# Performance work log

Measured on AMD Instinct MI355X. Metric: run time of the kernel, lower is better.

## Reference

```python
import jax, jax.numpy as jnp
import numpy as np

B, TOK, NT = 64, 64, 456          # batch, token_encoder_dim, num gene tokens
T = NT * TOK                      # flat gene_exp dim = 29184
D, H, NL = 256, 8, 4              # d_model, nhead, num_layers
HD = D // H                       # head_dim = 32
FF = 4 * D                        # ffn hidden
PH = 32                           # attention-pooling hidden
L = NT + 1                        # seq len incl. CLS token
LN_EPS = 1e-5
BN_EPS = 1e-5


def build_alibi_slopes(n_heads):
    # faithful to FlashAttentionBlock.build_alibi_slopes (base=2.0)
    return jnp.array([1.0 / 2.0 ** (i // (n_heads / 2.0)) for i in range(n_heads)],
                     dtype=jnp.float32)


def _ln(x, g, b):
    m = jnp.mean(x, axis=-1, keepdims=True)
    v = jnp.mean(jnp.square(x - m), axis=-1, keepdims=True)
    return (x - m) * jax.lax.rsqrt(v + LN_EPS) * g + b


def setup_inputs() -> dict:
    key = jax.random.key(0)
    ks = jax.random.split(key, 24)
    s = 0.02
    return {
        "gene_exp": jax.random.normal(ks[0], (B, T), dtype=jnp.float32),
        "coords": jax.random.normal(ks[1], (B, 3), dtype=jnp.float32),
        "w_in": jax.random.normal(ks[2], (TOK, D)) * s,
        "b_in": jnp.zeros((D,), jnp.float32),
        "w_cls": jax.random.normal(ks[3], (3, D)) * s,
        "b_cls": jnp.zeros((D,), jnp.float32),
        "qkv_w": jax.random.normal(ks[4], (NL, D, 3 * D)) * s,
        "qkv_b": jnp.zeros((NL, 3 * D), jnp.float32),
        "ln1_g": jnp.ones((NL, D), jnp.float32),
        "ln1_b": jnp.zeros((NL, D), jnp.float32),
        "ffn_w1": jax.random.normal(ks[5], (NL, D, FF)) * s,
        "ffn_b1": jnp.zeros((NL, FF), jnp.float32),
        "ffn_w2": jax.random.normal(ks[6], (NL, FF, D)) * s,
        "ffn_b2": jnp.zeros((NL, D), jnp.float32),
        "ln2_g": jnp.ones((NL, D), jnp.float32),
        "ln2_b": jnp.zeros((NL, D), jnp.float32),
        "th1_w": jax.random.normal(ks[7], (D, PH)) * s,
        "th1_b": jnp.zeros((PH,), jnp.float32),
        "bn_g": jnp.ones((PH,), jnp.float32),
        "bn_b": jnp.zeros((PH,), jnp.float32),
        "th2_w": jax.random.normal(ks[8], (PH, 1)) * s,
        "th2_b": jnp.zeros((1,), jnp.float32),
    }


def reference(gene_exp, coords, w_in, b_in, w_cls, b_cls, qkv_w, qkv_b,
              ln1_g, ln1_b, ffn_w1, ffn_b1, ffn_w2, ffn_b2, ln2_g, ln2_b,
              th1_w, th1_b, bn_g, bn_b, th2_w, th2_b):
    # tokenize gene expression + project
    x = gene_exp.reshape(B, NT, TOK) @ w_in + b_in            # [B, NT, D]
    cls = (coords @ w_cls + b_cls)[:, None, :]                # [B, 1, D]
    x = jnp.concatenate([cls, x], axis=1)                     # [B, L, D]

    # ALiBi bias: -slope_h * |i - j| (non-causal flash-attn convention)
    slopes = build_alibi_slopes(H)                            # [H]
    pos = jnp.arange(L, dtype=jnp.float32)
    bias = -slopes[:, None, None] * jnp.abs(pos[:, None] - pos[None, :])  # [H,L,L]

    scale = 1.0 / np.sqrt(HD)
    for l in range(NL):
        residual = x
        qkv = (x @ qkv_w[l] + qkv_b[l]).reshape(B, L, 3, H, HD)
        q, k, v = qkv[:, :, 0], qkv[:, :, 1], qkv[:, :, 2]    # [B, L, H, HD]
        scores = jnp.einsum('bihd,bjhd->bhij', q, k) * scale + bias
        attn = jax.nn.softmax(scores, axis=-1)                # [B, H, L, L]
        out = jnp.einsum('bhij,bjhd->bihd', attn, v).reshape(B, L, D)
        x = _ln(residual + out, ln1_g[l], ln1_b[l])
        residual = x
        h = jax.nn.relu(x @ ffn_w1[l] + ffn_b1[l]) @ ffn_w2[l] + ffn_b2[l]
        x = _ln(residual + h, ln2_g[l], ln2_b[l])

    # AttentionPooling (BatchNorm1d in eval mode: running mean 0, var 1)
    h = x @ th1_w + th1_b                                     # [B, L, PH]
    h = h * (bn_g / np.sqrt(1.0 + BN_EPS)) + bn_b
    scores = jax.nn.gelu(h) @ th2_w + th2_b                   # [B, L, 1]
    attn_w = jax.nn.softmax(scores, axis=1)[..., 0]           # [B, L]
    pooled = jnp.einsum('bl,bld->bd', attn_w, x)              # [B, D]
    return pooled
```

## Files before the change

### kernel.cpp

```cpp
#include <hip/hip_runtime.h>
#include <math.h>

#define B_   64
#define TOK_ 64
#define NT_  456
#define L_   457
#define D_   256
#define H_   8
#define HD_  32
#define FF_  1024
#define NL_  4
#define PH_  32
#define MPAD 29440

typedef unsigned int uint;
typedef unsigned short ushort;
typedef __bf16 v8bf __attribute__((ext_vector_type(8)));
typedef __bf16 v4bf __attribute__((ext_vector_type(4)));
typedef short v4s __attribute__((ext_vector_type(4)));
typedef float v4f __attribute__((ext_vector_type(4)));

__device__ __forceinline__ float bu2f(ushort x) {
    return __uint_as_float(((uint)x) << 16);
}
__device__ __forceinline__ ushort f2bu(float f) {
    union { float f; uint u; } x; x.f = f;
    uint r = (x.u + 0x7fffu + ((x.u >> 16) & 1u)) >> 16;
    return (ushort)r;
}
__device__ __forceinline__ uint pack_bf2(float a, float b) {
#if defined(__HIP_DEVICE_COMPILE__) && __has_builtin(__builtin_amdgcn_cvt_pk_bf16_f32)
    typedef __bf16 bf2v __attribute__((ext_vector_type(2)));
    bf2v v = __builtin_amdgcn_cvt_pk_bf16_f32(a, b);
    return *(uint*)&v;
#else
    return (uint)f2bu(a) | ((uint)f2bu(b) << 16);
#endif
}

__device__ __forceinline__ v4f mfma16(uint2 a, uint2 b, v4f c) {
#if defined(__HIP_DEVICE_COMPILE__)
#if __has_builtin(__builtin_amdgcn_mfma_f32_16x16x16_bf16)
    return __builtin_amdgcn_mfma_f32_16x16x16_bf16(*(v4bf*)&a, *(v4bf*)&b, c, 0, 0, 0);
#else
    return __builtin_amdgcn_mfma_f32_16x16x16bf16_1k(*(v4s*)&a, *(v4s*)&b, c, 0, 0, 0);
#endif
#else
    (void)a; (void)b;
    return c;
#endif
}

__device__ __forceinline__ void gload16(const void* g, void* l) {
    __builtin_amdgcn_global_load_lds(
        (const __attribute__((address_space(1))) void*)(unsigned long long)(uintptr_t)g,
        (__attribute__((address_space(3))) void*)(uint)(uintptr_t)l,
        16, 0, 0);
}

__global__ __launch_bounds__(512, 2) void mfma_gemm8(
    const ushort* __restrict__ A, const ushort* __restrict__ WT,
    const float* __restrict__ bias, ushort* __restrict__ Cout,
    int N, int K, int relu)
{
    __shared__ ushort lds[36864];

    const int NK = K >> 5;

    int nwg = gridDim.x, orig = blockIdx.x;
    int qd = nwg >> 3, rd = nwg & 7;
    int xcd = orig & 7, wi = orig >> 3;
    int wgid = (xcd < rd ? xcd * (qd + 1) : rd * (qd + 1) + (xcd - rd) * qd) + wi;
    int nCB = N >> 7;
    int colblk = (wgid % nCB) << 7;
    int rowblk = (wgid / nCB) << 8;

    int tid = threadIdx.x;
    int wave = tid >> 6, lane = tid & 63;
    int wm = wave >> 1, wn = wave & 1;
    int fr = lane & 15, fq = lane >> 4;

    const ushort* srcA0; const ushort* srcA1; const ushort* srcB0;
    {
        int idx = tid;
        int c = idx >> 3, G = (idx & 7) ^ (c & 7);
        srcA0 = A + (size_t)(rowblk + c * 2 + (G >> 2)) * K + (G & 3) * 8;
        idx = 512 + tid;
        c = idx >> 3; G = (idx & 7) ^ (c & 7);
        srcA1 = A + (size_t)(rowblk + c * 2 + (G >> 2)) * K + (G & 3) * 8;
        idx = tid;
        c = idx >> 3; G = (idx & 7) ^ (c & 7);
        srcB0 = WT + (size_t)(colblk + c * 2 + (G >> 2)) * K + (G & 3) * 8;
    }
    int duA0 = (wave * 64) * 8;
    int duA1 = (512 + wave * 64) * 8;
    int duB  = (wave * 64) * 8;

    int aoff[4], boff[4];
#pragma unroll
    for (int i = 0; i < 4; ++i) {
        int rl = wm * 64 + i * 16 + fr;
        int c = rl >> 1;
        aoff[i] = c * 64 + ((((rl & 1) * 4 + fq) ^ (c & 7)) * 8);
        rl = wn * 64 + i * 16 + fr;
        c = rl >> 1;
        boff[i] = c * 64 + ((((rl & 1) * 4 + fq) ^ (c & 7)) * 8);
    }

    v4f acc[4][4];
#pragma unroll
    for (int i = 0; i < 4; ++i)
#pragma unroll
        for (int j = 0; j < 4; ++j) acc[i][j] = (v4f)0.0f;

#pragma unroll
    for (int t = 0; t < 2; ++t) {
        ushort* pa = lds + t * 8192;
        ushort* pb = lds + 24576 + t * 4096;
        gload16(srcA0 + t * 32, pa + duA0);
        gload16(srcA1 + t * 32, pa + duA1);
        gload16(srcB0 + t * 32, pb + duB);
    }

    for (int t = 0; t < NK; ++t) {
        int slot = t % 3, pslot = (t + 2) % 3;
        const ushort* As = lds + slot * 8192;
        const ushort* Bs = lds + 24576 + slot * 4096;

        if (t < NK - 1) asm volatile("s_waitcnt vmcnt(3)" ::: "memory");
        else            asm volatile("s_waitcnt vmcnt(0)" ::: "memory");
        __builtin_amdgcn_s_barrier();
        asm volatile("" ::: "memory");

        if (t + 2 < NK) {
            ushort* pa = lds + pslot * 8192;
            ushort* pb = lds + 24576 + pslot * 4096;
            gload16(srcA0 + (t + 2) * 32, pa + duA0);
            gload16(srcA1 + (t + 2) * 32, pa + duA1);
            gload16(srcB0 + (t + 2) * 32, pb + duB);
        }

        v8bf av[4], bw[4];
#pragma unroll
        for (int i = 0; i < 4; ++i) av[i] = *(const v8bf*)(As + aoff[i]);
#pragma unroll
        for (int i = 0; i < 4; ++i) bw[i] = *(const v8bf*)(Bs + boff[i]);

        __builtin_amdgcn_s_setprio(1);
#pragma unroll
        for (int mi = 0; mi < 4; ++mi)
#pragma unroll
            for (int ni = 0; ni < 4; ++ni)
                acc[mi][ni] = __builtin_amdgcn_mfma_f32_16x16x32_bf16(
                    av[mi], bw[ni], acc[mi][ni], 0, 0, 0);
        __builtin_amdgcn_s_setprio(0);
    }

    __syncthreads();
    {
        const int PIT = 136;
#pragma unroll
        for (int ni = 0; ni < 4; ++ni) {
            int col = wn * 64 + ni * 16 + fr;
            float bv = bias[colblk + col];
#pragma unroll
            for (int mi = 0; mi < 4; ++mi) {
                int row0 = wm * 64 + mi * 16 + fq * 4;
#pragma unroll
                for (int r2 = 0; r2 < 4; ++r2) {
                    float v = acc[mi][ni][r2] + bv;
                    if (relu) v = fmaxf(v, 0.f);
                    lds[(row0 + r2) * PIT + col] = f2bu(v);
                }
            }
        }
        __syncthreads();
#pragma unroll
        for (int i = 0; i < 8; ++i) {
            int u = tid + 512 * i;
            int row = u >> 4, c8 = (u & 15) * 8;
            uint4 val = *(const uint4*)&lds[row * PIT + c8];
            *(uint4*)(Cout + (size_t)(rowblk + row) * N + colblk + c8) = val;
        }
    }
}

__global__ __launch_bounds__(512, 4) void ffn_kernel(
    const ushort* __restrict__ X, const ushort* __restrict__ W1P,
    const ushort* __restrict__ W2P, const float* __restrict__ b1,
    const float* __restrict__ b2, ushort* __restrict__ Out)
{
    __shared__ ushort Xs[16384];
    __shared__ ushort Hs[64 * 264];

    int r0 = blockIdx.x * 64;
    int tid = threadIdx.x;
    int wave = tid >> 6, lane = tid & 63;
    int fr = lane & 15, fq = lane >> 4;

#pragma unroll
    for (int i = 0; i < 4; ++i) {
        int u = tid + 512 * i;
        int kt = u >> 8, loc = u & 255;
        int c = loc >> 3, G = (loc & 7) ^ (c & 7);
        gload16(X + (size_t)(r0 + c * 2 + (G >> 2)) * 256 + kt * 32 + (G & 3) * 8,
                Xs + (size_t)kt * 2048 + (size_t)loc * 8);
    }

    int aoffs[4];
#pragma unroll
    for (int mi = 0; mi < 4; ++mi) {
        int ar = mi * 16 + fr, c = ar >> 1;
        aoffs[mi] = c * 64 + ((((ar & 1) * 4 + fq) ^ (c & 7)) * 8);
    }
    int wm2 = wave >> 2, wn2 = wave & 3;

    v4f acc2[2][4];
#pragma unroll
    for (int i = 0; i < 2; ++i)
#pragma unroll
        for (int j = 0; j < 4; ++j) acc2[i][j] = (v4f)0.0f;

    asm volatile("s_waitcnt vmcnt(0)" ::: "memory");
    __syncthreads();

#pragma unroll
    for (int q = 0; q < 4; ++q) {
        v4f acc1[4][2];
#pragma unroll
        for (int i = 0; i < 4; ++i)
#pragma unroll
            for (int j = 0; j < 2; ++j) acc1[i][j] = (v4f)0.0f;

        const ushort* w1p = W1P + (size_t)((q * 16 + wave * 2) * 8) * 64 * 8;
#pragma unroll
        for (int kc = 0; kc < 8; ++kc) {
            v8bf bf0 = *(const v8bf*)(w1p + ((size_t)kc * 64 + lane) * 8);
            v8bf bf1 = *(const v8bf*)(w1p + ((size_t)(8 + kc) * 64 + lane) * 8);
            v8bf a[4];
#pragma unroll
            for (int mi = 0; mi < 4; ++mi)
                a[mi] = *(const v8bf*)(Xs + kc * 2048 + aoffs[mi]);
#pragma unroll
            for (int mi = 0; mi < 4; ++mi) {
                acc1[mi][0] = __builtin_amdgcn_mfma_f32_16x16x32_bf16(
                    a[mi], bf0, acc1[mi][0], 0, 0, 0);
                acc1[mi][1] = __builtin_amdgcn_mfma_f32_16x16x32_bf16(
                    a[mi], bf1, acc1[mi][1], 0, 0, 0);
            }
        }
        float b1v[2];
#pragma unroll
        for (int ni = 0; ni < 2; ++ni)
            b1v[ni] = b1[q * 256 + wave * 32 + ni * 16 + fr];

        if (q) __syncthreads();
#pragma unroll
        for (int ni = 0; ni < 2; ++ni) {
            int col = wave * 32 + ni * 16 + fr;
#pragma unroll
            for (int mi = 0; mi < 4; ++mi) {
                int row0 = mi * 16 + fq * 4;
#pragma unroll
                for (int r2 = 0; r2 < 4; ++r2)
                    Hs[(row0 + r2) * 264 + col] =
                        f2bu(fmaxf(acc1[mi][ni][r2] + b1v[ni], 0.f));
            }
        }
        __syncthreads();

#pragma unroll
        for (int kk = 0; kk < 8; ++kk) {
            v8bf bw2[4];
#pragma unroll
            for (int ni = 0; ni < 4; ++ni)
                bw2[ni] = *(const v8bf*)(W2P +
                    (size_t)((((wn2 * 4 + ni) * 32 + q * 8 + kk) * 64 + lane)) * 8);
            v8bf a2[2];
#pragma unroll
            for (int mi = 0; mi < 2; ++mi)
                a2[mi] = *(const v8bf*)(Hs +
                    (wm2 * 32 + mi * 16 + fr) * 264 + kk * 32 + fq * 8);
#pragma unroll
            for (int mi = 0; mi < 2; ++mi)
#pragma unroll
                for (int ni = 0; ni < 4; ++ni)
                    acc2[mi][ni] = __builtin_amdgcn_mfma_f32_16x16x32_bf16(
                        a2[mi], bw2[ni], acc2[mi][ni], 0, 0, 0);
        }
    }

    __syncthreads();
    {
        float b2v[4];
#pragma unroll
        for (int ni = 0; ni < 4; ++ni) b2v[ni] = b2[wn2 * 64 + ni * 16 + fr];
#pragma unroll
        for (int ni = 0; ni < 4; ++ni) {
            int col = wn2 * 64 + ni * 16 + fr;
#pragma unroll
            for (int mi = 0; mi < 2; ++mi) {
                int row0 = wm2 * 32 + mi * 16 + fq * 4;
#pragma unroll
                for (int r2 = 0; r2 < 4; ++r2)
                    Hs[(row0 + r2) * 264 + col] = f2bu(acc2[mi][ni][r2] + b2v[ni]);
            }
        }
        __syncthreads();
#pragma unroll
        for (int i = 0; i < 4; ++i) {
            int u = tid + 512 * i;
            int row = u >> 5, c8 = (u & 31) * 8;
            *(uint4*)(Out + (size_t)(r0 + row) * 256 + c8) =
                *(const uint4*)&Hs[row * 264 + c8];
        }
    }
}

__global__ __launch_bounds__(256) void wpack_kernel(
    const float* __restrict__ W, ushort* __restrict__ P, int K, int N)
{
    int KC = K >> 5;
    int total = (N >> 4) * KC * 64;
    const float* Wl = W + (size_t)blockIdx.z * K * N;
    ushort* Pl = P + (size_t)blockIdx.z * K * N;
    int gid = blockIdx.x * 256 + threadIdx.x;
    if (gid >= total) return;
    int lane = gid & 63;
    int t = gid >> 6;
    int kc = t % KC, grp = t / KC;
    int n = grp * 16 + (lane & 15);
    int k0 = kc * 32 + (lane >> 4) * 8;
    float v[8];
#pragma unroll
    for (int e = 0; e < 8; ++e) v[e] = Wl[(size_t)(k0 + e) * N + n];
    uint4 o;
    o.x = pack_bf2(v[0], v[1]);
    o.y = pack_bf2(v[2], v[3]);
    o.z = pack_bf2(v[4], v[5]);
    o.w = pack_bf2(v[6], v[7]);
    *(uint4*)&Pl[(size_t)gid * 8] = o;
}

__global__ __launch_bounds__(256) void wcast_kernel(
    const float* __restrict__ W, ushort* __restrict__ WT, int K, int N)
{
    __shared__ float t[32][33];
    const float* Wl = W + (size_t)blockIdx.z * K * N;
    ushort* WTl = WT + (size_t)blockIdx.z * K * N;
    int n0 = blockIdx.x * 32, k0 = blockIdx.y * 32;
    int tx = threadIdx.x, ty = threadIdx.y;
#pragma unroll
    for (int r = 0; r < 32; r += 8)
        t[ty + r][tx] = Wl[(size_t)(k0 + ty + r) * N + n0 + tx];
    __syncthreads();
#pragma unroll
    for (int r = 0; r < 32; r += 8)
        WTl[(size_t)(n0 + ty + r) * K + k0 + tx] = f2bu(t[tx][ty + r]);
}

__global__ __launch_bounds__(256) void sgemm_kernel(
    const float* __restrict__ A, const float* __restrict__ W,
    const float* __restrict__ bias, ushort* __restrict__ Cb,
    int M, int N, int K)
{
    __shared__ float As_[16][64];
    __shared__ float Bs_[16][64];
    int tid = threadIdx.x;
    int rowblk = blockIdx.y * 64;
    int colblk = blockIdx.x * 64;
    int a_row = tid & 63, a_q = tid >> 6;
    int b_kr = tid >> 4, b_cg = tid & 15;
    int rm = tid >> 4, cn = tid & 15;
    float acc[4][4] = {};
    const float* Aptr = A + (size_t)(rowblk + a_row) * K;
    for (int kt = 0; kt < K; kt += 16) {
        float4 av = *(const float4*)(Aptr + kt + a_q * 4);
        float4 bv = *(const float4*)(W + (size_t)(kt + b_kr) * N + colblk + b_cg * 4);
        As_[a_q * 4 + 0][a_row] = av.x;
        As_[a_q * 4 + 1][a_row] = av.y;
        As_[a_q * 4 + 2][a_row] = av.z;
        As_[a_q * 4 + 3][a_row] = av.w;
        *(float4*)&Bs_[b_kr][b_cg * 4] = bv;
        __syncthreads();
#pragma unroll
        for (int kk = 0; kk < 16; ++kk) {
            float4 a4 = *(const float4*)&As_[kk][rm * 4];
            float4 b4 = *(const float4*)&Bs_[kk][cn * 4];
            float ar[4] = {a4.x, a4.y, a4.z, a4.w};
            float br[4] = {b4.x, b4.y, b4.z, b4.w};
#pragma unroll
            for (int i = 0; i < 4; ++i)
#pragma unroll
                for (int j = 0; j < 4; ++j) acc[i][j] += ar[i] * br[j];
        }
        __syncthreads();
    }
    float4 bv = *(const float4*)(bias + colblk + cn * 4);
    float bb[4] = {bv.x, bv.y, bv.z, bv.w};
#pragma unroll
    for (int i = 0; i < 4; ++i) {
        int grow = rowblk + rm * 4 + i;
        size_t orow = (size_t)(grow + grow / NT_ + 1);
        ushort4 h;
        h.x = f2bu(acc[i][0] + bb[0]);
        h.y = f2bu(acc[i][1] + bb[1]);
        h.z = f2bu(acc[i][2] + bb[2]);
        h.w = f2bu(acc[i][3] + bb[3]);
        *(ushort4*)(Cb + orow * N + colblk + cn * 4) = h;
    }
}

__global__ __launch_bounds__(256) void cls_kernel(
    const float* __restrict__ coords, const float* __restrict__ w_cls,
    const float* __restrict__ b_cls, ushort* __restrict__ Xb)
{
    int b = blockIdx.x;
    int t = threadIdx.x;
    float c0 = coords[b * 3 + 0], c1 = coords[b * 3 + 1], c2 = coords[b * 3 + 2];
    float v = c0 * w_cls[t] + c1 * w_cls[D_ + t] + c2 * w_cls[2 * D_ + t] + b_cls[t];
    Xb[(size_t)b * L_ * D_ + t] = f2bu(v);
}

__global__ __launch_bounds__(512) void attn_kernel(
    const ushort* __restrict__ qkv, ushort* __restrict__ out)
{
    __shared__ __align__(16) ushort Ks[464][40];
    __shared__ __align__(16) ushort Vt[32][488];

    int h = blockIdx.x, b = blockIdx.y;
    int tid = threadIdx.x;
    int wave = tid >> 6, lane = tid & 63;
    int fr = lane & 15, fq = lane >> 4;
    const float scale2 = 0.17677669529663687f * 1.4426950408889634f;
    float slope2 = ((h < 4) ? 1.0f : 0.5f) * 1.4426950408889634f;
    int W = (h < 4) ? 32 : 64;
    const ushort* base = qkv + (size_t)b * L_ * 768;

    for (int j = tid >> 2; j < 464; j += 128) {
        int c8 = (tid & 3) * 8;
        uint4 u = make_uint4(0u, 0u, 0u, 0u);
        if (j < L_) u = *(const uint4*)(base + (size_t)j * 768 + 256 + h * 32 + c8);
        *(uint4*)&Ks[j][c8] = u;
    }
    for (int m = wave; m < 32; m += 8) {
        int dg = (m >> 3) * 8, jb = m & 7;
        int j = jb * 64 + lane;
        uint4 u = make_uint4(0u, 0u, 0u, 0u);
        if (j < L_) u = *(const uint4*)(base + (size_t)j * 768 + 512 + h * 32 + dg);
        if (j < 488) {
            const ushort* pu = (const ushort*)&u;
#pragma unroll
            for (int e = 0; e < 8; ++e) Vt[dg + e][j] = pu[e];
        }
    }
    __syncthreads();

    for (int pr = wave; pr < 15; pr += 8) {
        int q0 = pr * 32;
        int twoB = (pr < 14);
        int kclo = max(0, (q0 - W) >> 5);
        int kchi = min(13, (q0 + 31 + W) >> 5);
        int doTail = (q0 + 31 + W >= 448);
        uint4 quA = *(const uint4*)(base + (size_t)(q0 + fr) * 768 + h * 32 + fq * 8);
        v8bf qfA = *(v8bf*)&quA;
        uint4 quB = *(const uint4*)(base + (size_t)(q0 + 16 + fr) * 768 + h * 32 + fq * 8);
        v8bf qfB = *(v8bf*)&quB;
        float fqAq = (float)(q0 + fr);
        float fqBq = fqAq + 16.0f;
        float psA = 0.f, psB = 0.f;
        v4f oA0 = (v4f)0.0f, oA1 = (v4f)0.0f, oB0 = (v4f)0.0f, oB1 = (v4f)0.0f;

        for (int kc = kclo; kc <= kchi; ++kc) {
            int kb = kc * 32;
            v8bf kf0 = *(const v8bf*)&Ks[kb + fr][fq * 8];
            v8bf kf1 = *(const v8bf*)&Ks[kb + 16 + fr][fq * 8];
            uint2 va0 = *(const uint2*)&Vt[fr][kb + fq * 4];
            uint2 va1 = *(const uint2*)&Vt[16 + fr][kb + fq * 4];
            uint2 vb0 = *(const uint2*)&Vt[fr][kb + 16 + fq * 4];
            uint2 vb1 = *(const uint2*)&Vt[16 + fr][kb + 16 + fq * 4];
            float ke = (float)(kb + 4 * fq);

            v4f dA0 = (v4f)0.0f, dA1 = (v4f)0.0f;
            dA0 = __builtin_amdgcn_mfma_f32_16x16x32_bf16(kf0, qfA, dA0, 0, 0, 0);
            dA1 = __builtin_amdgcn_mfma_f32_16x16x32_bf16(kf1, qfA, dA1, 0, 0, 0);
            {
                float dl0 = fqAq - ke, dl1 = dl0 - 16.0f;
                float pe[4], po[4];
#pragma unroll
                for (int r = 0; r < 4; ++r) {
                    pe[r] = exp2f(fmaf(dA0[r], scale2, -slope2 * fabsf(dl0 - (float)r)));
                    po[r] = exp2f(fmaf(dA1[r], scale2, -slope2 * fabsf(dl1 - (float)r)));
                    psA += pe[r] + po[r];
                }
                uint2 ue, uo;
                ue.x = pack_bf2(pe[0], pe[1]); ue.y = pack_bf2(pe[2], pe[3]);
                uo.x = pack_bf2(po[0], po[1]); uo.y = pack_bf2(po[2], po[3]);
                oA0 = mfma16(va0, ue, oA0);
                oA1 = mfma16(va1, ue, oA1);
                oA0 = mfma16(vb0, uo, oA0);
                oA1 = mfma16(vb1, uo, oA1);
            }
            if (twoB) {
                v4f dB0 = (v4f)0.0f, dB1 = (v4f)0.0f;
                dB0 = __builtin_amdgcn_mfma_f32_16x16x32_bf16(kf0, qfB, dB0, 0, 0, 0);
                dB1 = __builtin_amdgcn_mfma_f32_16x16x32_bf16(kf1, qfB, dB1, 0, 0, 0);
                float dl0 = fqBq - ke, dl1 = dl0 - 16.0f;
                float pe[4], po[4];
#pragma unroll
                for (int r = 0; r < 4; ++r) {
                    pe[r] = exp2f(fmaf(dB0[r], scale2, -slope2 * fabsf(dl0 - (float)r)));
                    po[r] = exp2f(fmaf(dB1[r], scale2, -slope2 * fabsf(dl1 - (float)r)));
                    psB += pe[r] + po[r];
                }
                uint2 ue, uo;
                ue.x = pack_bf2(pe[0], pe[1]); ue.y = pack_bf2(pe[2], pe[3]);
                uo.x = pack_bf2(po[0], po[1]); uo.y = pack_bf2(po[2], po[3]);
                oB0 = mfma16(va0, ue, oB0);
                oB1 = mfma16(va1, ue, oB1);
                oB0 = mfma16(vb0, uo, oB0);
                oB1 = mfma16(vb1, uo, oB1);
            }
        }
        if (doTail) {
            v8bf kf0 = *(const v8bf*)&Ks[448 + fr][fq * 8];
            uint2 va0 = *(const uint2*)&Vt[fr][448 + fq * 4];
            uint2 va1 = *(const uint2*)&Vt[16 + fr][448 + fq * 4];
            v4f dA0 = (v4f)0.0f;
            dA0 = __builtin_amdgcn_mfma_f32_16x16x32_bf16(kf0, qfA, dA0, 0, 0, 0);
            float pe[4];
#pragma unroll
            for (int r = 0; r < 4; ++r) {
                int k = 448 + 4 * fq + r;
                pe[r] = (k < L_)
                    ? exp2f(fmaf(dA0[r], scale2, -slope2 * fabsf(fqAq - (float)k))) : 0.f;
                psA += pe[r];
            }
            uint2 ue;
            ue.x = pack_bf2(pe[0], pe[1]); ue.y = pack_bf2(pe[2], pe[3]);
            oA0 = mfma16(va0, ue, oA0);
            oA1 = mfma16(va1, ue, oA1);
            if (twoB) {
                v4f dB0 = (v4f)0.0f;
                dB0 = __builtin_amdgcn_mfma_f32_16x16x32_bf16(kf0, qfB, dB0, 0, 0, 0);
                float pf[4];
#pragma unroll
                for (int r = 0; r < 4; ++r) {
                    int k = 448 + 4 * fq + r;
                    pf[r] = (k < L_)
                        ? exp2f(fmaf(dB0[r], scale2, -slope2 * fabsf(fqBq - (float)k))) : 0.f;
                    psB += pf[r];
                }
                uint2 ub;
                ub.x = pack_bf2(pf[0], pf[1]); ub.y = pack_bf2(pf[2], pf[3]);
                oB0 = mfma16(va0, ub, oB0);
                oB1 = mfma16(va1, ub, oB1);
            }
        }

        psA += __shfl_xor(psA, 16);
        psA += __shfl_xor(psA, 32);
        psB += __shfl_xor(psB, 16);
        psB += __shfl_xor(psB, 32);
        {
            int q = q0 + fr;
            if (q < L_) {
                float inv = 1.0f / psA;
                uint2 w0, w1;
                w0.x = pack_bf2(oA0[0] * inv, oA0[1] * inv);
                w0.y = pack_bf2(oA0[2] * inv, oA0[3] * inv);
                w1.x = pack_bf2(oA1[0] * inv, oA1[1] * inv);
                w1.y = pack_bf2(oA1[2] * inv, oA1[3] * inv);
                ushort* op = out + (size_t)(b * L_ + q) * D_ + h * 32;
                *(uint2*)(op + fq * 4) = w0;
                *(uint2*)(op + 16 + fq * 4) = w1;
            }
        }
        if (twoB) {
            int q = q0 + 16 + fr;
            if (q < L_) {
                float inv = 1.0f / psB;
                uint2 w0, w1;
                w0.x = pack_bf2(oB0[0] * inv, oB0[1] * inv);
                w0.y = pack_bf2(oB0[2] * inv, oB0[3] * inv);
                w1.x = pack_bf2(oB1[0] * inv, oB1[1] * inv);
                w1.y = pack_bf2(oB1[2] * inv, oB1[3] * inv);
                ushort* op = out + (size_t)(b * L_ + q) * D_ + h * 32;
                *(uint2*)(op + fq * 4) = w0;
                *(uint2*)(op + 16 + fq * 4) = w1;
            }
        }
    }
}

__global__ __launch_bounds__(256) void ln_kernel(
    const ushort* __restrict__ res, const ushort* __restrict__ y,
    const float* __restrict__ g, const float* __restrict__ bb,
    ushort* __restrict__ xbout)
{
    int row = blockIdx.x * 4 + (threadIdx.x >> 6);
    int lane = threadIdx.x & 63;
    size_t off = (size_t)row * D_ + lane * 4;
    ushort4 rv4 = *(const ushort4*)(res + off);
    ushort4 yv4 = *(const ushort4*)(y + off);
    float4 v;
    v.x = bu2f(rv4.x) + bu2f(yv4.x);
    v.y = bu2f(rv4.y) + bu2f(yv4.y);
    v.z = bu2f(rv4.z) + bu2f(yv4.z);
    v.w = bu2f(rv4.w) + bu2f(yv4.w);

    float s = v.x + v.y + v.z + v.w;
#pragma unroll
    for (int o = 1; o < 64; o <<= 1) s += __shfl_xor(s, o);
    float mean = s * (1.0f / 256.0f);

    float4 d;
    d.x = v.x - mean; d.y = v.y - mean; d.z = v.z - mean; d.w = v.w - mean;
    float sq = d.x * d.x + d.y * d.y + d.z * d.z + d.w * d.w;
#pragma unroll
    for (int o = 1; o < 64; o <<= 1) sq += __shfl_xor(sq, o);
    float rstd = rsqrtf(sq * (1.0f / 256.0f) + 1e-5f);

    float4 gv = *(const float4*)(g + lane * 4);
    float4 bv = *(const float4*)(bb + lane * 4);
    ushort4 hb;
    hb.x = f2bu(d.x * rstd * gv.x + bv.x);
    hb.y = f2bu(d.y * rstd * gv.y + bv.y);
    hb.z = f2bu(d.z * rstd * gv.z + bv.z);
    hb.w = f2bu(d.w * rstd * gv.w + bv.w);
    *(ushort4*)(xbout + off) = hb;
}

__global__ __launch_bounds__(256) void head1_kernel(
    const ushort* __restrict__ Xb, const ushort* __restrict__ th1T,
    const float* __restrict__ b1, const float* __restrict__ bng,
    const float* __restrict__ bnb, const float* __restrict__ w2,
    const float* __restrict__ b2, float* __restrict__ SCp)
{
    __shared__ ushort As[128 * 32];
    __shared__ ushort Bs[32 * 264];
    int tid = threadIdx.x;
    int wave = tid >> 6, lane = tid & 63;
    int fr = lane & 15, fq = lane >> 4;
    int rowblk = blockIdx.x * 128;
    int scol = fq ^ (lane & 3) ^ ((lane >> 2) & 1);

    for (int i = tid; i < 1024; i += 256) {
        int r = i >> 5, c8 = (i & 31) * 8;
        *(uint4*)&Bs[r * 264 + c8] = *(const uint4*)(th1T + r * 256 + c8);
    }

    int c0 = wave * 64 + lane;
    int r0 = c0 >> 2, k0g = (c0 & 3) ^ (r0 & 3) ^ ((r0 >> 2) & 1);
    int c1 = 256 + c0;
    int r1 = c1 >> 2, k1g = (c1 & 3) ^ (r1 & 3) ^ ((r1 >> 2) & 1);
    const ushort* Ag0 = Xb + (size_t)(rowblk + r0) * 256 + k0g * 8;
    const ushort* Ag1 = Xb + (size_t)(rowblk + r1) * 256 + k1g * 8;
    ushort* lA0 = As + (size_t)(wave * 64) * 8;
    ushort* lA1 = As + (size_t)(256 + wave * 64) * 8;

    v4f acc[2][2];
#pragma unroll
    for (int i = 0; i < 2; ++i)
#pragma unroll
        for (int j = 0; j < 2; ++j) acc[i][j] = (v4f)0.0f;

    for (int kt = 0; kt < 256; kt += 32) {
        gload16(Ag0 + kt, lA0);
        gload16(Ag1 + kt, lA1);
        __syncthreads();
        v8bf a[2], bfr[2];
#pragma unroll
        for (int mi = 0; mi < 2; ++mi)
            a[mi] = *(const v8bf*)(As + (size_t)((wave * 2 + mi) * 16 + fr) * 32 + scol * 8);
#pragma unroll
        for (int ni = 0; ni < 2; ++ni)
            bfr[ni] = *(const v8bf*)(Bs + (size_t)(ni * 16 + fr) * 264 + kt + fq * 8);
#pragma unroll
        for (int mi = 0; mi < 2; ++mi)
#pragma unroll
            for (int ni = 0; ni < 2; ++ni)
                acc[mi][ni] = __builtin_amdgcn_mfma_f32_16x16x32_bf16(
                    a[mi], bfr[ni], acc[mi][ni], 0, 0, 0);
        __syncthreads();
    }

    const float bnr = 0.9999950000374997f;
    float b1v[2], bsv[2], bbv[2], w2v[2];
#pragma unroll
    for (int ni = 0; ni < 2; ++ni) {
        int j = ni * 16 + fr;
        b1v[ni] = b1[j];
        bsv[ni] = bng[j] * bnr;
        bbv[ni] = bnb[j];
        w2v[ni] = w2[j];
    }
    const float gc = 0.7978845608028654f;
    float b2v = b2[0];
#pragma unroll
    for (int mi = 0; mi < 2; ++mi) {
#pragma unroll
        for (int r = 0; r < 4; ++r) {
            float s = 0.f;
#pragma unroll
            for (int ni = 0; ni < 2; ++ni) {
                float hb = (acc[mi][ni][r] + b1v[ni]) * bsv[ni] + bbv[ni];
                float t = tanhf(gc * (hb + 0.044715f * hb * hb * hb));
                s += 0.5f * hb * (1.0f + t) * w2v[ni];
            }
#pragma unroll
            for (int o = 1; o < 16; o <<= 1) s += __shfl_xor(s, o);
            int row = rowblk + (wave * 2 + mi) * 16 + fq * 4 + r;
            if (fr == 0 && row < B_ * L_) SCp[row] = s + b2v;
        }
    }
}

__global__ __launch_bounds__(256) void head2_kernel(
    const float* __restrict__ SCp, const ushort* __restrict__ Xb,
    float* __restrict__ outp)
{
    int cg = blockIdx.x, b = blockIdx.y;
    int tid = threadIdx.x;
    __shared__ float wbuf[L_];
    __shared__ float r1[4], r2[4];
    __shared__ float part[4][64];
    const float* s = SCp + (size_t)b * L_;

    float m = -1e30f;
    for (int j = tid; j < L_; j += 256) m = fmaxf(m, s[j]);
#pragma unroll
    for (int o = 1; o < 64; o <<= 1) m = fmaxf(m, __shfl_xor(m, o));
    if ((tid & 63) == 0) r1[tid >> 6] = m;
    __syncthreads();
    m = fmaxf(fmaxf(r1[0], r1[1]), fmaxf(r1[2], r1[3]));

    float sum = 0.f;
    for (int j = tid; j < L_; j += 256) {
        float e = __expf(s[j] - m);
        wbuf[j] = e;
        sum += e;
    }
#pragma unroll
    for (int o = 1; o < 64; o <<= 1) sum += __shfl_xor(sum, o);
    if ((tid & 63) == 0) r2[tid >> 6] = sum;
    __syncthreads();
    float inv = 1.0f / (r2[0] + r2[1] + r2[2] + r2[3]);

    int c = tid & 63, pt = tid >> 6;
    int col = cg * 64 + c;
    float acc = 0.f;
    const ushort* xb = Xb + (size_t)b * L_ * D_ + col;
    for (int l = pt; l < L_; l += 4) acc += wbuf[l] * bu2f(xb[(size_t)l * D_]);
    part[pt][c] = acc;
    __syncthreads();
    if (pt == 0)
        outp[b * D_ + col] = (part[0][c] + part[1][c] + part[2][c] + part[3][c]) * inv;
}

extern "C" void kernel_launch(void* const* d_in, const int* in_sizes, int n_in,
                              void* d_out, int out_size, void* d_ws, size_t ws_size,
                              hipStream_t stream)
{
    const float* gene   = (const float*)d_in[0];
    const float* coords = (const float*)d_in[1];
    const float* w_in   = (const float*)d_in[2];
    const float* b_in   = (const float*)d_in[3];
    const float* w_cls  = (const float*)d_in[4];
    const float* b_cls  = (const float*)d_in[5];
    const float* qkv_w  = (const float*)d_in[6];
    const float* qkv_b  = (const float*)d_in[7];
    const float* ln1_g  = (const float*)d_in[8];
    const float* ln1_b  = (const float*)d_in[9];
    const float* ffn_w1 = (const float*)d_in[10];
    const float* ffn_b1 = (const float*)d_in[11];
    const float* ffn_w2 = (const float*)d_in[12];
    const float* ffn_b2 = (const float*)d_in[13];
    const float* ln2_g  = (const float*)d_in[14];
    const float* ln2_b  = (const float*)d_in[15];
    const float* th1_w  = (const float*)d_in[16];
    const float* th1_b  = (const float*)d_in[17];
    const float* bn_g   = (const float*)d_in[18];
    const float* bn_b   = (const float*)d_in[19];
    const float* th2_w  = (const float*)d_in[20];
    const float* th2_b  = (const float*)d_in[21];
    float* out = (float*)d_out;

    const int ROWS = B_ * L_;
    char* p = (char*)d_ws;
    ushort* AOb  = (ushort*)p; p += (size_t)MPAD * 256 * 2;
    ushort* Xb   = (ushort*)p; p += (size_t)MPAD * 256 * 2;
    ushort* SH   = (ushort*)p; p += (size_t)MPAD * 1024 * 2;
    ushort* qkvT = (ushort*)p; p += (size_t)NL_ * 768 * 256 * 2;
    ushort* W1P  = (ushort*)p; p += (size_t)NL_ * 1024 * 256 * 2;
    ushort* W2P  = (ushort*)p; p += (size_t)NL_ * 256 * 1024 * 2;
    ushort* th1T = (ushort*)p; p += (size_t)32 * 256 * 2;
    float*  SCp  = (float*)p;  p += (size_t)ROWS * 4;

    const int RB2 = MPAD / 256;

    wcast_kernel<<<dim3(768 / 32, 256 / 32, NL_), dim3(32, 8), 0, stream>>>(qkv_w, qkvT, 256, 768);
    wpack_kernel<<<dim3(128, 1, NL_), 256, 0, stream>>>(ffn_w1, W1P, 256, 1024);
    wpack_kernel<<<dim3(128, 1, NL_), 256, 0, stream>>>(ffn_w2, W2P, 1024, 256);
    wcast_kernel<<<dim3(1, 8, 1), dim3(32, 8), 0, stream>>>(th1_w, th1T, 256, 32);

    sgemm_kernel<<<dim3(D_ / 64, (B_ * NT_) / 64), 256, 0, stream>>>(
        gene, w_in, b_in, Xb, B_ * NT_, D_, TOK_);
    cls_kernel<<<B_, 256, 0, stream>>>(coords, w_cls, b_cls, Xb);

    for (int l = 0; l < NL_; ++l) {
        mfma_gemm8<<<RB2 * (768 / 128), 512, 0, stream>>>(
            Xb, qkvT + (size_t)l * 768 * 256, qkv_b + l * 768, SH, 768, 256, 0);
        attn_kernel<<<dim3(H_, B_), 512, 0, stream>>>(SH, AOb);
        ln_kernel<<<ROWS / 4, 256, 0, stream>>>(Xb, AOb, ln1_g + l * D_, ln1_b + l * D_, Xb);
        ffn_kernel<<<MPAD / 64, 512, 0, stream>>>(
            Xb, W1P + (size_t)l * 1024 * 256, W2P + (size_t)l * 256 * 1024,
            ffn_b1 + l * 1024, ffn_b2 + l * D_, AOb);
        ln_kernel<<<ROWS / 4, 256, 0, stream>>>(Xb, AOb, ln2_g + l * D_, ln2_b + l * D_, Xb);
    }

    head1_kernel<<<MPAD / 128, 256, 0, stream>>>(
        Xb, th1T, th1_b, bn_g, bn_b, th2_w, th2_b, SCp);
    head2_kernel<<<dim3(4, B_), 256, 0, stream>>>(SCp, Xb, out);
}
```

Measured before the change: 640.2 us.

## Fuse both LayerNorms into the FFN kernel prologue and epilogue

The residual-add + LayerNorm1 now runs inside the FFN kernel prologue, writing the normalized rows straight into the swizzled LDS tile. The FFN output then goes through residual-add + LayerNorm2 in the epilogue, reusing that LDS copy as the residual. This drops two separate LN launches per layer and their global round trips of intermediate activations. In exchange the FFN kernel does more scalar work and shuffle reductions, and it writes Xb in place, which depends on each block reading only its own rows.

```diff
diff --git a/kernel.cpp b/kernel.cpp
--- a/kernel.cpp
+++ b/kernel.cpp
@@ -186,9 +186,12 @@
 }
 
 __global__ __launch_bounds__(512, 4) void ffn_kernel(
-    const ushort* __restrict__ X, const ushort* __restrict__ W1P,
-    const ushort* __restrict__ W2P, const float* __restrict__ b1,
-    const float* __restrict__ b2, ushort* __restrict__ Out)
+    const ushort* __restrict__ Xres, const ushort* __restrict__ AO,
+    const float* __restrict__ l1g, const float* __restrict__ l1b,
+    const ushort* __restrict__ W1P, const ushort* __restrict__ W2P,
+    const float* __restrict__ b1, const float* __restrict__ b2,
+    const float* __restrict__ l2g, const float* __restrict__ l2b,
+    ushort* __restrict__ Xout)
 {
     __shared__ ushort Xs[16384];
     __shared__ ushort Hs[64 * 264];
@@ -198,20 +201,51 @@
     int wave = tid >> 6, lane = tid & 63;
     int fr = lane & 15, fq = lane >> 4;
 
-#pragma unroll
-    for (int i = 0; i < 4; ++i) {
-        int u = tid + 512 * i;
-        int kt = u >> 8, loc = u & 255;
-        int c = loc >> 3, G = (loc & 7) ^ (c & 7);
-        gload16(X + (size_t)(r0 + c * 2 + (G >> 2)) * 256 + kt * 32 + (G & 3) * 8,
-                Xs + (size_t)kt * 2048 + (size_t)loc * 8);
+    {
+        float4 g1 = *(const float4*)(l1g + lane * 4);
+        float4 be1 = *(const float4*)(l1b + lane * 4);
+        ushort4 xr[8], ar[8];
+#pragma unroll
+        for (int rr = 0; rr < 8; ++rr) {
+            size_t off = (size_t)(r0 + wave * 8 + rr) * 256 + lane * 4;
+            xr[rr] = *(const ushort4*)(Xres + off);
+            ar[rr] = *(const ushort4*)(AO + off);
+        }
+#pragma unroll
+        for (int rr = 0; rr < 8; ++rr) {
+            int row = wave * 8 + rr;
+            float4 v;
+            v.x = bu2f(xr[rr].x) + bu2f(ar[rr].x);
+            v.y = bu2f(xr[rr].y) + bu2f(ar[rr].y);
+            v.z = bu2f(xr[rr].z) + bu2f(ar[rr].z);
+            v.w = bu2f(xr[rr].w) + bu2f(ar[rr].w);
+            float s = v.x + v.y + v.z + v.w;
+#pragma unroll
+            for (int o = 1; o < 64; o <<= 1) s += __shfl_xor(s, o);
+            float mean = s * (1.0f / 256.0f);
+            float4 d;
+            d.x = v.x - mean; d.y = v.y - mean; d.z = v.z - mean; d.w = v.w - mean;
+            float sq = d.x * d.x + d.y * d.y + d.z * d.z + d.w * d.w;
+#pragma unroll
+            for (int o = 1; o < 64; o <<= 1) sq += __shfl_xor(sq, o);
+            float rstd = rsqrtf(sq * (1.0f / 256.0f) + 1e-5f);
+            ushort4 hb;
+            hb.x = f2bu(d.x * rstd * g1.x + be1.x);
+            hb.y = f2bu(d.y * rstd * g1.y + be1.y);
+            hb.z = f2bu(d.z * rstd * g1.z + be1.z);
+            hb.w = f2bu(d.w * rstd * g1.w + be1.w);
+            int kt = lane >> 3, g = (lane >> 1) & 3, c = row >> 1;
+            int Gp = ((row & 1) * 4 + g) ^ (c & 7);
+            int addr = kt * 2048 + (c * 8 + Gp) * 8 + (lane & 1) * 4;
+            *(uint2*)&Xs[addr] = *(uint2*)&hb;
+        }
     }
 
     int aoffs[4];
 #pragma unroll
     for (int mi = 0; mi < 4; ++mi) {
-        int ar = mi * 16 + fr, c = ar >> 1;
-        aoffs[mi] = c * 64 + ((((ar & 1) * 4 + fq) ^ (c & 7)) * 8);
+        int ar2 = mi * 16 + fr, c = ar2 >> 1;
+        aoffs[mi] = c * 64 + ((((ar2 & 1) * 4 + fq) ^ (c & 7)) * 8);
     }
     int wm2 = wave >> 2, wn2 = wave & 3;
 
@@ -221,7 +255,6 @@
 #pragma unroll
         for (int j = 0; j < 4; ++j) acc2[i][j] = (v4f)0.0f;
 
-    asm volatile("s_waitcnt vmcnt(0)" ::: "memory");
     __syncthreads();
 
 #pragma unroll
@@ -307,12 +340,39 @@
             }
         }
         __syncthreads();
-#pragma unroll
-        for (int i = 0; i < 4; ++i) {
-            int u = tid + 512 * i;
-            int row = u >> 5, c8 = (u & 31) * 8;
-            *(uint4*)(Out + (size_t)(r0 + row) * 256 + c8) =
-                *(const uint4*)&Hs[row * 264 + c8];
+
+        float4 g2 = *(const float4*)(l2g + lane * 4);
+        float4 be2 = *(const float4*)(l2b + lane * 4);
+#pragma unroll
+        for (int rr = 0; rr < 8; ++rr) {
+            int row = wave * 8 + rr;
+            ushort4 cv = *(const ushort4*)&Hs[row * 264 + lane * 4];
+            int kt = lane >> 3, g = (lane >> 1) & 3, c = row >> 1;
+            int Gp = ((row & 1) * 4 + g) ^ (c & 7);
+            int addr = kt * 2048 + (c * 8 + Gp) * 8 + (lane & 1) * 4;
+            uint2 uu = *(const uint2*)&Xs[addr];
+            ushort4 uv = *(ushort4*)&uu;
+            float4 v;
+            v.x = bu2f(cv.x) + bu2f(uv.x);
+            v.y = bu2f(cv.y) + bu2f(uv.y);
+            v.z = bu2f(cv.z) + bu2f(uv.z);
+            v.w = bu2f(cv.w) + bu2f(uv.w);
+            float s = v.x + v.y + v.z + v.w;
+#pragma unroll
+            for (int o = 1; o < 64; o <<= 1) s += __shfl_xor(s, o);
+            float mean = s * (1.0f / 256.0f);
+            float4 d;
+            d.x = v.x - mean; d.y = v.y - mean; d.z = v.z - mean; d.w = v.w - mean;
+            float sq = d.x * d.x + d.y * d.y + d.z * d.z + d.w * d.w;
+#pragma unroll
+            for (int o = 1; o < 64; o <<= 1) sq += __shfl_xor(sq, o);
+            float rstd = rsqrtf(sq * (1.0f / 256.0f) + 1e-5f);
+            ushort4 hb;
+            hb.x = f2bu(d.x * rstd * g2.x + be2.x);
+            hb.y = f2bu(d.y * rstd * g2.y + be2.y);
+            hb.z = f2bu(d.z * rstd * g2.z + be2.z);
+            hb.w = f2bu(d.w * rstd * g2.w + be2.w);
+            *(ushort4*)(Xout + (size_t)(r0 + row) * 256 + lane * 4) = hb;
         }
     }
 }
@@ -591,44 +651,6 @@
             }
         }
     }
-}
-
-__global__ __launch_bounds__(256) void ln_kernel(
-    const ushort* __restrict__ res, const ushort* __restrict__ y,
-    const float* __restrict__ g, const float* __restrict__ bb,
-    ushort* __restrict__ xbout)
-{
-    int row = blockIdx.x * 4 + (threadIdx.x >> 6);
-    int lane = threadIdx.x & 63;
-    size_t off = (size_t)row * D_ + lane * 4;
-    ushort4 rv4 = *(const ushort4*)(res + off);
-    ushort4 yv4 = *(const ushort4*)(y + off);
-    float4 v;
-    v.x = bu2f(rv4.x) + bu2f(yv4.x);
-    v.y = bu2f(rv4.y) + bu2f(yv4.y);
-    v.z = bu2f(rv4.z) + bu2f(yv4.z);
-    v.w = bu2f(rv4.w) + bu2f(yv4.w);
-
-    float s = v.x + v.y + v.z + v.w;
-#pragma unroll
-    for (int o = 1; o < 64; o <<= 1) s += __shfl_xor(s, o);
-    float mean = s * (1.0f / 256.0f);
-
-    float4 d;
-    d.x = v.x - mean; d.y = v.y - mean; d.z = v.z - mean; d.w = v.w - mean;
-    float sq = d.x * d.x + d.y * d.y + d.z * d.z + d.w * d.w;
-#pragma unroll
-    for (int o = 1; o < 64; o <<= 1) sq += __shfl_xor(sq, o);
-    float rstd = rsqrtf(sq * (1.0f / 256.0f) + 1e-5f);
-
-    float4 gv = *(const float4*)(g + lane * 4);
-    float4 bv = *(const float4*)(bb + lane * 4);
-    ushort4 hb;
-    hb.x = f2bu(d.x * rstd * gv.x + bv.x);
-    hb.y = f2bu(d.y * rstd * gv.y + bv.y);
-    hb.z = f2bu(d.z * rstd * gv.z + bv.z);
-    hb.w = f2bu(d.w * rstd * gv.w + bv.w);
-    *(ushort4*)(xbout + off) = hb;
 }
 
 __global__ __launch_bounds__(256) void head1_kernel(
@@ -812,11 +834,11 @@
         mfma_gemm8<<<RB2 * (768 / 128), 512, 0, stream>>>(
             Xb, qkvT + (size_t)l * 768 * 256, qkv_b + l * 768, SH, 768, 256, 0);
         attn_kernel<<<dim3(H_, B_), 512, 0, stream>>>(SH, AOb);
-        ln_kernel<<<ROWS / 4, 256, 0, stream>>>(Xb, AOb, ln1_g + l * D_, ln1_b + l * D_, Xb);
         ffn_kernel<<<MPAD / 64, 512, 0, stream>>>(
-            Xb, W1P + (size_t)l * 1024 * 256, W2P + (size_t)l * 256 * 1024,
-            ffn_b1 + l * 1024, ffn_b2 + l * D_, AOb);
-        ln_kernel<<<ROWS / 4, 256, 0, stream>>>(Xb, AOb, ln2_g + l * D_, ln2_b + l * D_, Xb);
+            Xb, AOb, ln1_g + l * D_, ln1_b + l * D_,
+            W1P + (size_t)l * 1024 * 256, W2P + (size_t)l * 256 * 1024,
+            ffn_b1 + l * 1024, ffn_b2 + l * D_,
+            ln2_g + l * D_, ln2_b + l * D_, Xb);
     }
 
     head1_kernel<<<MPAD / 128, 256, 0, stream>>>(
```

Result: faster. 627.2 us (median of 3 runs) (-2.0%).
